# Kernel optimization log

Hardware: AMD Instinct MI355X
Metric: run time of the kernel (lower is better)

Reference implementation:

```python
import jax, jax.numpy as jnp
import numpy as np

LEVELS = 2
BS = 8                 # block_size == plane_h == plane_w
NORMALS = (0, 1, 2)    # axis-aligned plane normals within each block
TAU = 0.05
INV_SQRT2 = 0.7071067811865476

# ---------- 1D orthonormal Haar along an axis ----------

def _dwt1(x, axis):
    x = jnp.moveaxis(x, axis, -1)
    a, b = x[..., 0::2], x[..., 1::2]
    lo = (a + b) * INV_SQRT2
    hi = (a - b) * INV_SQRT2
    return jnp.moveaxis(lo, -1, axis), jnp.moveaxis(hi, -1, axis)


def _idwt1(lo, hi, axis):
    lo = jnp.moveaxis(lo, axis, -1)
    hi = jnp.moveaxis(hi, axis, -1)
    even = (lo + hi) * INV_SQRT2
    odd = (lo - hi) * INV_SQRT2
    y = jnp.stack([even, odd], axis=-1).reshape(lo.shape[:-1] + (lo.shape[-1] * 2,))
    return jnp.moveaxis(y, -1, axis)

# ---------- one level of separable 3D Haar (8 subbands) ----------

def _dwt3_level(x):
    ld, hd = _dwt1(x, -3)
    out = {}
    for dn, db in (('l', ld), ('h', hd)):
        lh, hh = _dwt1(db, -2)
        for hn, hb in (('l', lh), ('h', hh)):
            lw, hw = _dwt1(hb, -1)
            out[dn + hn + 'l'] = lw
            out[dn + hn + 'h'] = hw
    return out


def _idwt3_level(bands):
    rec_h = {dn + hn: _idwt1(bands[dn + hn + 'l'], bands[dn + hn + 'h'], -1)
             for dn in 'lh' for hn in 'lh'}
    rec_d = {dn: _idwt1(rec_h[dn + 'l'], rec_h[dn + 'h'], -2) for dn in 'lh'}
    return _idwt1(rec_d['l'], rec_d['h'], -3)

# ---------- full multi-level 2D Haar on the last two dims (planes) ----------

def _haar2_fwd(p):
    s = p.shape[-1]
    out = p
    while s > 1:
        sub = out[..., :s, :s]
        a, b = sub[..., 0::2, :], sub[..., 1::2, :]
        sub = jnp.concatenate([(a + b) * INV_SQRT2, (a - b) * INV_SQRT2], axis=-2)
        a, b = sub[..., :, 0::2], sub[..., :, 1::2]
        sub = jnp.concatenate([(a + b) * INV_SQRT2, (a - b) * INV_SQRT2], axis=-1)
        out = out.at[..., :s, :s].set(sub)
        s //= 2
    return out


def _haar2_inv(c):
    s_full = c.shape[-1]
    out = c
    s = 2
    while s <= s_full:
        sub = out[..., :s, :s]
        lo, hi = sub[..., :, :s // 2], sub[..., :, s // 2:]
        even = (lo + hi) * INV_SQRT2
        odd = (lo - hi) * INV_SQRT2
        sub = jnp.stack([even, odd], axis=-1).reshape(sub.shape[:-1] + (s,))
        lo, hi = sub[..., :s // 2, :], sub[..., s // 2:, :]
        even = (lo + hi) * INV_SQRT2
        odd = (lo - hi) * INV_SQRT2
        sub = jnp.stack([even, odd], axis=-2).reshape(sub.shape[:-2] + (s, s))
        out = out.at[..., :s, :s].set(sub)
        s *= 2
    return out

# ---------- block extraction / assembly ----------

def _extract_blocks(band, bs):
    B, C, D, H, W = band.shape
    pd, ph, pw = (-D) % bs, (-H) % bs, (-W) % bs
    band = jnp.pad(band, ((0, 0), (0, 0), (0, pd), (0, ph), (0, pw)), mode='edge')
    nd, nh, nw = (D + pd) // bs, (H + ph) // bs, (W + pw) // bs
    blk = band.reshape(B, C, nd, bs, nh, bs, nw, bs).transpose(0, 1, 2, 4, 6, 3, 5, 7)
    return blk.reshape(-1, bs, bs, bs), (B, C, D, H, W), (nd, nh, nw)


def _assemble_blocks(blocks, orig, nblk, bs):
    B, C, D, H, W = orig
    nd, nh, nw = nblk
    x = blocks.reshape(B, C, nd, nh, nw, bs, bs, bs).transpose(0, 1, 2, 5, 3, 6, 4, 7)
    x = x.reshape(B, C, nd * bs, nh * bs, nw * bs)
    return x[:, :, :D, :H, :W]

# ---------- planewise bandlet analysis / synthesis ----------

def _analyze(blocks):
    # for each normal axis n: slice cube into planes perpendicular to n, 2D Haar each plane
    return jnp.stack([_haar2_fwd(jnp.moveaxis(blocks, 1 + n, 1)) for n in NORMALS], axis=1)


def _synthesize(packed):
    recs = [jnp.moveaxis(_haar2_inv(packed[:, i]), 1, 1 + n) for i, n in enumerate(NORMALS)]
    acc = recs[0]
    for r in recs[1:]:
        acc = acc + r
    return acc / len(NORMALS)


def _soft_threshold(c, tau):
    dc = c[..., 0, 0]  # keep per-plane DC coefficient
    t = jnp.sign(c) * jnp.maximum(jnp.abs(c) - tau, 0.0)
    return t.at[..., 0, 0].set(dc)

# ---------- full encode -> threshold -> reconstruct ----------

def _forward(x):
    B, C, D, H, W = x.shape
    mult = 2 ** LEVELS
    pd, ph, pw = (-D) % mult, (-H) % mult, (-W) % mult
    xp = jnp.pad(x, ((0, 0), (0, 0), (0, pd), (0, ph), (0, pw)), mode='reflect')
    approx = xp
    levels = []
    for _ in range(LEVELS):
        bands = _dwt3_level(approx)
        approx = bands.pop('lll')
        levels.append(bands)
    rec_levels = []
    for bands in levels:
        rec = {}
        for name, band in bands.items():
            blocks, orig, nblk = _extract_blocks(band, BS)
            packed = _soft_threshold(_analyze(blocks), TAU)
            rec[name] = _assemble_blocks(_synthesize(packed), orig, nblk, BS)
        rec_levels.append(rec)
    y = approx
    for bands in reversed(rec_levels):
        bands = dict(bands)
        bands['lll'] = y
        y = _idwt3_level(bands)
    return y[:, :, :D, :H, :W]


def setup_inputs() -> dict:
    key = jax.random.key(0)
    x = jax.random.normal(key, (2, 1, 160, 160, 160), dtype=jnp.float32)
    return {"x": x}


def reference(x):
    return _forward(x)
```

## Files before the change

kernel.cpp:

```cpp
#include <hip/hip_runtime.h>

#define IS2 0.7071067811865476f
#define C3F 0.35355339059327373f
#define TAU_F 0.05f

__device__ __forceinline__ void haar2_fwd(float (&m)[64]) {
    float t[64];
    #pragma unroll
    for (int half = 4; half >= 1; half >>= 1) {
        const int sz = half * 2;
        #pragma unroll
        for (int r = 0; r < half; ++r)
            #pragma unroll
            for (int c = 0; c < sz; ++c) {
                float a = m[(2*r)*8 + c], b = m[(2*r+1)*8 + c];
                t[r*8 + c]        = (a + b) * IS2;
                t[(r+half)*8 + c] = (a - b) * IS2;
            }
        #pragma unroll
        for (int r = 0; r < sz; ++r)
            #pragma unroll
            for (int c = 0; c < sz; ++c) m[r*8+c] = t[r*8+c];
        #pragma unroll
        for (int r = 0; r < sz; ++r)
            #pragma unroll
            for (int c = 0; c < half; ++c) {
                float a = m[r*8 + 2*c], b = m[r*8 + 2*c + 1];
                t[r*8 + c]        = (a + b) * IS2;
                t[r*8 + c + half] = (a - b) * IS2;
            }
        #pragma unroll
        for (int r = 0; r < sz; ++r)
            #pragma unroll
            for (int c = 0; c < sz; ++c) m[r*8+c] = t[r*8+c];
    }
}

__device__ __forceinline__ void haar2_inv(float (&m)[64]) {
    float t[64];
    #pragma unroll
    for (int sz = 2; sz <= 8; sz <<= 1) {
        const int half = sz >> 1;
        #pragma unroll
        for (int r = 0; r < sz; ++r)
            #pragma unroll
            for (int c = 0; c < half; ++c) {
                float lo = m[r*8 + c], hi = m[r*8 + c + half];
                t[r*8 + 2*c]     = (lo + hi) * IS2;
                t[r*8 + 2*c + 1] = (lo - hi) * IS2;
            }
        #pragma unroll
        for (int r = 0; r < sz; ++r)
            #pragma unroll
            for (int c = 0; c < sz; ++c) m[r*8+c] = t[r*8+c];
        #pragma unroll
        for (int r = 0; r < half; ++r)
            #pragma unroll
            for (int c = 0; c < sz; ++c) {
                float lo = m[r*8 + c], hi = m[(r+half)*8 + c];
                t[(2*r)*8 + c]   = (lo + hi) * IS2;
                t[(2*r+1)*8 + c] = (lo - hi) * IS2;
            }
        #pragma unroll
        for (int r = 0; r < sz; ++r)
            #pragma unroll
            for (int c = 0; c < sz; ++c) m[r*8+c] = t[r*8+c];
    }
}

__device__ __forceinline__ void bandlet_slice(float (&m)[64]) {
    haar2_fwd(m);
    float dc = m[0];
    #pragma unroll
    for (int e = 0; e < 64; ++e) {
        float v = m[e];
        float av = fabsf(v) - TAU_F;
        m[e] = av > 0.0f ? copysignf(av, v) : 0.0f;
    }
    m[0] = dc;
    haar2_inv(m);
}

template<int S, int B>
__global__ __launch_bounds__(256) void dwt3_fwd(const float* __restrict__ in,
                                                float* __restrict__ out) {
    const int tid = blockIdx.x * blockDim.x + threadIdx.x;
    constexpr int total = B * S * S * S;
    if (tid >= total) return;
    const int w = tid % S;
    const int h = (tid / S) % S;
    const int d = (tid / (S*S)) % S;
    const int b = tid / (S*S*S);
    constexpr int IS = 2 * S;
    const float* p = in + (((size_t)b * IS + 2*d) * IS + 2*h) * IS + 2*w;

    float2 q00 = *(const float2*)(p);
    float2 q01 = *(const float2*)(p + IS);
    float2 q10 = *(const float2*)(p + (size_t)IS*IS);
    float2 q11 = *(const float2*)(p + (size_t)IS*IS + IS);

    float wl00 = q00.x + q00.y, wh00 = q00.x - q00.y;
    float wl01 = q01.x + q01.y, wh01 = q01.x - q01.y;
    float wl10 = q10.x + q10.y, wh10 = q10.x - q10.y;
    float wl11 = q11.x + q11.y, wh11 = q11.x - q11.y;
    float hl0l = wl00 + wl01, hh0l = wl00 - wl01;
    float hl0h = wh00 + wh01, hh0h = wh00 - wh01;
    float hl1l = wl10 + wl11, hh1l = wl10 - wl11;
    float hl1h = wh10 + wh11, hh1h = wh10 - wh11;
    constexpr size_t bs_ = (size_t)B * S * S * S;
    const size_t o = (size_t)tid;
    out[0*bs_ + o] = (hl0l + hl1l) * C3F;
    out[1*bs_ + o] = (hl0h + hl1h) * C3F;
    out[2*bs_ + o] = (hh0l + hh1l) * C3F;
    out[3*bs_ + o] = (hh0h + hh1h) * C3F;
    out[4*bs_ + o] = (hl0l - hl1l) * C3F;
    out[5*bs_ + o] = (hl0h - hl1h) * C3F;
    out[6*bs_ + o] = (hh0l - hh1l) * C3F;
    out[7*bs_ + o] = (hh0h - hh1h) * C3F;
}

template<int S, int B>
__global__ __launch_bounds__(256) void dwt3_inv(const float* __restrict__ bands,
                                                float* __restrict__ out) {
    const int tid = blockIdx.x * blockDim.x + threadIdx.x;
    constexpr int total = B * S * S * S;
    if (tid >= total) return;
    const int w = tid % S;
    const int h = (tid / S) % S;
    const int d = (tid / (S*S)) % S;
    const int b = tid / (S*S*S);
    constexpr size_t bs_ = (size_t)B * S * S * S;
    const size_t o = (size_t)tid;

    float b0 = bands[0*bs_+o], b1 = bands[1*bs_+o], b2 = bands[2*bs_+o], b3 = bands[3*bs_+o];
    float b4 = bands[4*bs_+o], b5 = bands[5*bs_+o], b6 = bands[6*bs_+o], b7 = bands[7*bs_+o];
    float c0 = b0 + b4, c1 = b1 + b5, c2 = b2 + b6, c3 = b3 + b7;
    float c4 = b0 - b4, c5 = b1 - b5, c6 = b2 - b6, c7 = b3 - b7;
    float e00 = c0 + c2, e01 = c1 + c3;
    float e02 = c0 - c2, e03 = c1 - c3;
    float e10 = c4 + c6, e11 = c5 + c7;
    float e12 = c4 - c6, e13 = c5 - c7;
    constexpr int IS = 2 * S;
    float* p = out + (((size_t)b * IS + 2*d) * IS + 2*h) * IS + 2*w;
    *(float2*)(p)                        = make_float2((e00+e01)*C3F, (e00-e01)*C3F);
    *(float2*)(p + IS)                   = make_float2((e02+e03)*C3F, (e02-e03)*C3F);
    *(float2*)(p + (size_t)IS*IS)        = make_float2((e10+e11)*C3F, (e10-e11)*C3F);
    *(float2*)(p + (size_t)IS*IS + IS)   = make_float2((e12+e13)*C3F, (e12-e13)*C3F);
}

__global__ __launch_bounds__(64, 2) void blockproc2(float* __restrict__ b1,
                                                    float* __restrict__ b2) {
    constexpr int LST = 516;
    __shared__ __align__(16) float lin[8 * LST];

    const int t  = threadIdx.x;
    const int nb = t >> 3;
    const int s  = t & 7;
    const int wg = blockIdx.x;

    float* base; unsigned S, BPB, ND; int bid; bool valid;
    if (wg < 1750) { base = b1; S = 80; BPB = 2000; ND = 10; bid = wg*8 + nb; valid = true; }
    else           { base = b2; S = 40; BPB = 250;  ND = 5;  bid = (wg-1750)*8 + nb; valid = bid < 1750; }

    const unsigned S2 = S * S, S3 = S2 * S;
    const unsigned ub   = (unsigned)bid;
    const unsigned band = ub / BPB;
    const unsigned r0   = ub - band * BPB;
    const unsigned nd2  = ND * ND, nd3 = nd2 * ND;
    const unsigned bb   = r0 / nd3;
    const unsigned r1   = r0 - bb * nd3;
    const unsigned di   = r1 / nd2;
    const unsigned r2i  = r1 - di * nd2;
    const unsigned hi   = r2i / ND;
    const unsigned wi   = r2i - hi * ND;
    float* gp = base + (size_t)band * (size_t)(2u * S3) + (size_t)bb * S3
              + (size_t)(8u * di) * S2 + (size_t)(8u * hi) * S + 8u * wi;

    float* L = &lin[nb * LST];

    if (valid) {
        #pragma unroll
        for (int u = 0; u < 8; ++u) {
            const float* g0 = gp + u * S2 + s * S;
            float4 v0 = *(const float4*)(g0);
            float4 v1 = *(const float4*)(g0 + 4);
            *(float4*)&L[u*64 + s*8]     = v0;
            *(float4*)&L[u*64 + s*8 + 4] = v1;
        }
    }
    __syncthreads();

    float a[64], g[64], w[64];

    #pragma unroll
    for (int r = 0; r < 8; ++r) {
        float4 v0 = *(const float4*)&L[s*64 + r*8];
        float4 v1 = *(const float4*)&L[s*64 + r*8 + 4];
        a[r*8+0]=v0.x; a[r*8+1]=v0.y; a[r*8+2]=v0.z; a[r*8+3]=v0.w;
        a[r*8+4]=v1.x; a[r*8+5]=v1.y; a[r*8+6]=v1.z; a[r*8+7]=v1.w;
    }
    bandlet_slice(a);

    #pragma unroll
    for (int r = 0; r < 8; ++r)
        #pragma unroll
        for (int c = 0; c < 8; ++c)
            g[r*8+c] = L[r*64 + c*8 + s];
    bandlet_slice(g);

    #pragma unroll
    for (int r = 0; r < 8; ++r) {
        float4 v0 = *(const float4*)&L[r*64 + s*8];
        float4 v1 = *(const float4*)&L[r*64 + s*8 + 4];
        w[r*8+0]=v0.x; w[r*8+1]=v0.y; w[r*8+2]=v0.z; w[r*8+3]=v0.w;
        w[r*8+4]=v1.x; w[r*8+5]=v1.y; w[r*8+6]=v1.z; w[r*8+7]=v1.w;
    }
    __syncthreads();

    #pragma unroll
    for (int r = 0; r < 8; ++r)
        #pragma unroll
        for (int c = 0; c < 8; ++c)
            L[r*64 + c*8 + s] = g[r*8+c];

    bandlet_slice(w);

    __syncthreads();
    #pragma unroll
    for (int r = 0; r < 8; ++r) {
        float4 v0 = *(const float4*)&L[s*64 + r*8];
        float4 v1 = *(const float4*)&L[s*64 + r*8 + 4];
        a[r*8+0]+=v0.x; a[r*8+1]+=v0.y; a[r*8+2]+=v0.z; a[r*8+3]+=v0.w;
        a[r*8+4]+=v1.x; a[r*8+5]+=v1.y; a[r*8+6]+=v1.z; a[r*8+7]+=v1.w;
    }
    __syncthreads();
    #pragma unroll
    for (int r = 0; r < 8; ++r) {
        float4 v0 = make_float4(w[r*8+0], w[r*8+1], w[r*8+2], w[r*8+3]);
        float4 v1 = make_float4(w[r*8+4], w[r*8+5], w[r*8+6], w[r*8+7]);
        *(float4*)&L[r*64 + s*8]     = v0;
        *(float4*)&L[r*64 + s*8 + 4] = v1;
    }
    __syncthreads();
    #pragma unroll
    for (int r = 0; r < 8; ++r) {
        float4 v0 = *(const float4*)&L[s*64 + r*8];
        float4 v1 = *(const float4*)&L[s*64 + r*8 + 4];
        a[r*8+0]+=v0.x; a[r*8+1]+=v0.y; a[r*8+2]+=v0.z; a[r*8+3]+=v0.w;
        a[r*8+4]+=v1.x; a[r*8+5]+=v1.y; a[r*8+6]+=v1.z; a[r*8+7]+=v1.w;
    }

    if (valid) {
        #pragma unroll
        for (int j = 0; j < 8; ++j) {
            float4 o0 = make_float4(a[j*8+0]*(1.0f/3.0f), a[j*8+1]*(1.0f/3.0f),
                                    a[j*8+2]*(1.0f/3.0f), a[j*8+3]*(1.0f/3.0f));
            float4 o1 = make_float4(a[j*8+4]*(1.0f/3.0f), a[j*8+5]*(1.0f/3.0f),
                                    a[j*8+6]*(1.0f/3.0f), a[j*8+7]*(1.0f/3.0f));
            float* q = gp + s * S2 + j * S;
            *(float4*)(q)     = o0;
            *(float4*)(q + 4) = o1;
        }
    }
}

extern "C" void kernel_launch(void* const* d_in, const int* in_sizes, int n_in,
                              void* d_out, int out_size, void* d_ws, size_t ws_size,
                              hipStream_t stream) {
    const float* x = (const float*)d_in[0];
    float* out = (float*)d_out;
    float* bands1 = (float*)d_ws;
    float* bands2 = (float*)d_out;

    constexpr int B = 2;
    constexpr size_t B1S = (size_t)B * 80 * 80 * 80;
    constexpr size_t B2S = (size_t)B * 40 * 40 * 40;

    dwt3_fwd<80, B><<<(B*80*80*80) / 256, 256, 0, stream>>>(x, bands1);
    dwt3_fwd<40, B><<<(B*40*40*40) / 256, 256, 0, stream>>>(bands1, bands2);
    blockproc2<<<1750 + 219, 64, 0, stream>>>(bands1 + B1S, bands2 + B2S);
    dwt3_inv<40, B><<<(B*40*40*40) / 256, 256, 0, stream>>>(bands2, bands1);
    dwt3_inv<80, B><<<(B*80*80*80) / 256, 256, 0, stream>>>(bands1, out);
}
```

Before: 119.2 us.

## Fuse forward DWT with bandlet processing and collapse level-2 into one kernel

Level-1 forward Haar is fused with the bandlet thresholding of its seven detail bands in shared memory, so the detail bands are processed without a global round trip first. The whole level-2 path (forward DWT, bandlet processing, inverse DWT) becomes a single kernel operating in place on the LLL band. This cuts five launches to three and removes several full global-memory passes. The cost is small 64-thread workgroups with 7/8 lanes active in the bandlet stage, and only 250 workgroups for level 2, which may leave the GPU underoccupied.

```diff
diff --git a/kernel.cpp b/kernel.cpp
--- a/kernel.cpp
+++ b/kernel.cpp
@@ -81,55 +81,227 @@
     haar2_inv(m);
 }
 
-template<int S, int B>
-__global__ __launch_bounds__(256) void dwt3_fwd(const float* __restrict__ in,
-                                                float* __restrict__ out) {
+__device__ __forceinline__ void bandlet_core(float* __restrict__ L, int s,
+                                             bool valid, float (&a)[64]) {
+    float g[64], w[64];
+    if (valid) {
+        #pragma unroll
+        for (int r = 0; r < 8; ++r) {
+            float4 v0 = *(const float4*)&L[s*64 + r*8];
+            float4 v1 = *(const float4*)&L[s*64 + r*8 + 4];
+            a[r*8+0]=v0.x; a[r*8+1]=v0.y; a[r*8+2]=v0.z; a[r*8+3]=v0.w;
+            a[r*8+4]=v1.x; a[r*8+5]=v1.y; a[r*8+6]=v1.z; a[r*8+7]=v1.w;
+        }
+        bandlet_slice(a);
+        #pragma unroll
+        for (int r = 0; r < 8; ++r)
+            #pragma unroll
+            for (int c = 0; c < 8; ++c)
+                g[r*8+c] = L[r*64 + c*8 + s];
+        bandlet_slice(g);
+        #pragma unroll
+        for (int r = 0; r < 8; ++r) {
+            float4 v0 = *(const float4*)&L[r*64 + s*8];
+            float4 v1 = *(const float4*)&L[r*64 + s*8 + 4];
+            w[r*8+0]=v0.x; w[r*8+1]=v0.y; w[r*8+2]=v0.z; w[r*8+3]=v0.w;
+            w[r*8+4]=v1.x; w[r*8+5]=v1.y; w[r*8+6]=v1.z; w[r*8+7]=v1.w;
+        }
+    }
+    __syncthreads();
+    if (valid) {
+        #pragma unroll
+        for (int r = 0; r < 8; ++r)
+            #pragma unroll
+            for (int c = 0; c < 8; ++c)
+                L[r*64 + c*8 + s] = g[r*8+c];
+        bandlet_slice(w);
+    }
+    __syncthreads();
+    if (valid) {
+        #pragma unroll
+        for (int r = 0; r < 8; ++r) {
+            float4 v0 = *(const float4*)&L[s*64 + r*8];
+            float4 v1 = *(const float4*)&L[s*64 + r*8 + 4];
+            a[r*8+0]+=v0.x; a[r*8+1]+=v0.y; a[r*8+2]+=v0.z; a[r*8+3]+=v0.w;
+            a[r*8+4]+=v1.x; a[r*8+5]+=v1.y; a[r*8+6]+=v1.z; a[r*8+7]+=v1.w;
+        }
+    }
+    __syncthreads();
+    if (valid) {
+        #pragma unroll
+        for (int r = 0; r < 8; ++r) {
+            *(float4*)&L[r*64 + s*8]     = make_float4(w[r*8+0], w[r*8+1], w[r*8+2], w[r*8+3]);
+            *(float4*)&L[r*64 + s*8 + 4] = make_float4(w[r*8+4], w[r*8+5], w[r*8+6], w[r*8+7]);
+        }
+    }
+    __syncthreads();
+    if (valid) {
+        #pragma unroll
+        for (int r = 0; r < 8; ++r) {
+            float4 v0 = *(const float4*)&L[s*64 + r*8];
+            float4 v1 = *(const float4*)&L[s*64 + r*8 + 4];
+            a[r*8+0]+=v0.x; a[r*8+1]+=v0.y; a[r*8+2]+=v0.z; a[r*8+3]+=v0.w;
+            a[r*8+4]+=v1.x; a[r*8+5]+=v1.y; a[r*8+6]+=v1.z; a[r*8+7]+=v1.w;
+        }
+    }
+}
+
+__global__ __launch_bounds__(64, 2) void fwd1_bp(const float* __restrict__ x,
+                                                 float* __restrict__ bands) {
+    constexpr int LST = 516;
+    constexpr size_t B1S = (size_t)2 * 80 * 80 * 80;
+    __shared__ __align__(16) float lin[7 * LST];
+
+    const int t  = threadIdx.x;
+    const int wg = blockIdx.x;
+    const int b  = wg / 1000;
+    const int tl = wg - b * 1000;
+    const int td = tl / 100;
+    const int rr = tl - td * 100;
+    const int th = rr / 10;
+    const int tw = rr - th * 10;
+    const int j = t >> 3, w = t & 7;
+
+    const float* ip = x + ((size_t)(b*160 + 16*td)) * 25600 + (size_t)(16*th) * 160 + 16*tw;
+    float* lllp = bands + ((size_t)(b*80 + 8*td)) * 6400 + (size_t)(8*th) * 80 + 8*tw;
+
+    #pragma unroll
+    for (int q = 0; q < 8; ++q) {
+        const float* p = ip + (size_t)(2*q) * 25600 + (2*j) * 160 + 2*w;
+        float2 q00 = *(const float2*)(p);
+        float2 q01 = *(const float2*)(p + 160);
+        float2 q10 = *(const float2*)(p + 25600);
+        float2 q11 = *(const float2*)(p + 25600 + 160);
+        float wl00 = q00.x + q00.y, wh00 = q00.x - q00.y;
+        float wl01 = q01.x + q01.y, wh01 = q01.x - q01.y;
+        float wl10 = q10.x + q10.y, wh10 = q10.x - q10.y;
+        float wl11 = q11.x + q11.y, wh11 = q11.x - q11.y;
+        float hl0l = wl00 + wl01, hh0l = wl00 - wl01;
+        float hl0h = wh00 + wh01, hh0h = wh00 - wh01;
+        float hl1l = wl10 + wl11, hh1l = wl10 - wl11;
+        float hl1h = wh10 + wh11, hh1h = wh10 - wh11;
+        const int pos = q*64 + j*8 + w;
+        lin[0*LST + pos] = (hl0h + hl1h) * C3F;
+        lin[1*LST + pos] = (hh0l + hh1l) * C3F;
+        lin[2*LST + pos] = (hh0h + hh1h) * C3F;
+        lin[3*LST + pos] = (hl0l - hl1l) * C3F;
+        lin[4*LST + pos] = (hl0h - hl1h) * C3F;
+        lin[5*LST + pos] = (hh0l - hh1l) * C3F;
+        lin[6*LST + pos] = (hh0h - hh1h) * C3F;
+        lllp[q*6400 + j*80 + w] = (hl0l + hl1l) * C3F;
+    }
+    __syncthreads();
+
+    const int nbp = t >> 3, s = t & 7;
+    const bool valid = nbp < 7;
+    float a[64];
+    bandlet_core(&lin[(valid ? nbp : 0) * LST], s, valid, a);
+
+    if (valid) {
+        float* gp = bands + (size_t)(nbp + 1) * B1S
+                  + ((size_t)(b*80 + 8*td + s)) * 6400 + (size_t)(8*th) * 80 + 8*tw;
+        #pragma unroll
+        for (int jj = 0; jj < 8; ++jj) {
+            float* qo = gp + jj * 80;
+            *(float4*)(qo)     = make_float4(a[jj*8+0]*(1.0f/3.0f), a[jj*8+1]*(1.0f/3.0f),
+                                             a[jj*8+2]*(1.0f/3.0f), a[jj*8+3]*(1.0f/3.0f));
+            *(float4*)(qo + 4) = make_float4(a[jj*8+4]*(1.0f/3.0f), a[jj*8+5]*(1.0f/3.0f),
+                                             a[jj*8+6]*(1.0f/3.0f), a[jj*8+7]*(1.0f/3.0f));
+        }
+    }
+}
+
+__global__ __launch_bounds__(64, 2) void l2_pipeline(float* __restrict__ lll) {
+    constexpr int LST = 516;
+    __shared__ __align__(16) float lin[8 * LST];
+
+    const int t  = threadIdx.x;
+    const int wg = blockIdx.x;
+    const int b  = wg / 125;
+    const int tl = wg - b * 125;
+    const int td = tl / 25;
+    const int rr = tl - td * 25;
+    const int th = rr / 5;
+    const int tw = rr - th * 5;
+    const int j = t >> 3, w = t & 7;
+
+    float* base = lll + ((size_t)(b*80 + 16*td)) * 6400 + (size_t)(16*th) * 80 + 16*tw;
+
+    #pragma unroll
+    for (int q = 0; q < 8; ++q) {
+        const float* p = base + (size_t)(2*q) * 6400 + (2*j) * 80 + 2*w;
+        float2 q00 = *(const float2*)(p);
+        float2 q01 = *(const float2*)(p + 80);
+        float2 q10 = *(const float2*)(p + 6400);
+        float2 q11 = *(const float2*)(p + 6400 + 80);
+        float wl00 = q00.x + q00.y, wh00 = q00.x - q00.y;
+        float wl01 = q01.x + q01.y, wh01 = q01.x - q01.y;
+        float wl10 = q10.x + q10.y, wh10 = q10.x - q10.y;
+        float wl11 = q11.x + q11.y, wh11 = q11.x - q11.y;
+        float hl0l = wl00 + wl01, hh0l = wl00 - wl01;
+        float hl0h = wh00 + wh01, hh0h = wh00 - wh01;
+        float hl1l = wl10 + wl11, hh1l = wl10 - wl11;
+        float hl1h = wh10 + wh11, hh1h = wh10 - wh11;
+        const int pos = q*64 + j*8 + w;
+        lin[0*LST + pos] = (hl0l + hl1l) * C3F;
+        lin[1*LST + pos] = (hl0h + hl1h) * C3F;
+        lin[2*LST + pos] = (hh0l + hh1l) * C3F;
+        lin[3*LST + pos] = (hh0h + hh1h) * C3F;
+        lin[4*LST + pos] = (hl0l - hl1l) * C3F;
+        lin[5*LST + pos] = (hl0h - hl1h) * C3F;
+        lin[6*LST + pos] = (hh0l - hh1l) * C3F;
+        lin[7*LST + pos] = (hh0h - hh1h) * C3F;
+    }
+    __syncthreads();
+
+    const int nbp = t >> 3, s = t & 7;
+    const bool valid = nbp < 7;
+    float a[64];
+    bandlet_core(&lin[(valid ? nbp + 1 : 0) * LST], s, valid, a);
+
+    __syncthreads();
+    if (valid) {
+        float* L = &lin[(nbp + 1) * LST];
+        #pragma unroll
+        for (int jj = 0; jj < 8; ++jj) {
+            *(float4*)&L[s*64 + jj*8]     = make_float4(a[jj*8+0]*(1.0f/3.0f), a[jj*8+1]*(1.0f/3.0f),
+                                                        a[jj*8+2]*(1.0f/3.0f), a[jj*8+3]*(1.0f/3.0f));
+            *(float4*)&L[s*64 + jj*8 + 4] = make_float4(a[jj*8+4]*(1.0f/3.0f), a[jj*8+5]*(1.0f/3.0f),
+                                                        a[jj*8+6]*(1.0f/3.0f), a[jj*8+7]*(1.0f/3.0f));
+        }
+    }
+    __syncthreads();
+
+    #pragma unroll
+    for (int q = 0; q < 8; ++q) {
+        const int pos = q*64 + j*8 + w;
+        float b0 = lin[0*LST + pos], b1 = lin[1*LST + pos];
+        float b2 = lin[2*LST + pos], b3 = lin[3*LST + pos];
+        float b4 = lin[4*LST + pos], b5 = lin[5*LST + pos];
+        float b6 = lin[6*LST + pos], b7 = lin[7*LST + pos];
+        float c0 = b0 + b4, c1 = b1 + b5, c2 = b2 + b6, c3 = b3 + b7;
+        float c4 = b0 - b4, c5 = b1 - b5, c6 = b2 - b6, c7 = b3 - b7;
+        float e00 = c0 + c2, e01 = c1 + c3;
+        float e02 = c0 - c2, e03 = c1 - c3;
+        float e10 = c4 + c6, e11 = c5 + c7;
+        float e12 = c4 - c6, e13 = c5 - c7;
+        float* pp = base + (size_t)(2*q) * 6400 + (2*j) * 80 + 2*w;
+        *(float2*)(pp)             = make_float2((e00+e01)*C3F, (e00-e01)*C3F);
+        *(float2*)(pp + 80)        = make_float2((e02+e03)*C3F, (e02-e03)*C3F);
+        *(float2*)(pp + 6400)      = make_float2((e10+e11)*C3F, (e10-e11)*C3F);
+        *(float2*)(pp + 6400 + 80) = make_float2((e12+e13)*C3F, (e12-e13)*C3F);
+    }
+}
+
+__global__ __launch_bounds__(256) void dwt3_inv80(const float* __restrict__ bands,
+                                                  float* __restrict__ out) {
     const int tid = blockIdx.x * blockDim.x + threadIdx.x;
-    constexpr int total = B * S * S * S;
-    if (tid >= total) return;
+    constexpr int S = 80;
     const int w = tid % S;
     const int h = (tid / S) % S;
     const int d = (tid / (S*S)) % S;
     const int b = tid / (S*S*S);
-    constexpr int IS = 2 * S;
-    const float* p = in + (((size_t)b * IS + 2*d) * IS + 2*h) * IS + 2*w;
-
-    float2 q00 = *(const float2*)(p);
-    float2 q01 = *(const float2*)(p + IS);
-    float2 q10 = *(const float2*)(p + (size_t)IS*IS);
-    float2 q11 = *(const float2*)(p + (size_t)IS*IS + IS);
-
-    float wl00 = q00.x + q00.y, wh00 = q00.x - q00.y;
-    float wl01 = q01.x + q01.y, wh01 = q01.x - q01.y;
-    float wl10 = q10.x + q10.y, wh10 = q10.x - q10.y;
-    float wl11 = q11.x + q11.y, wh11 = q11.x - q11.y;
-    float hl0l = wl00 + wl01, hh0l = wl00 - wl01;
-    float hl0h = wh00 + wh01, hh0h = wh00 - wh01;
-    float hl1l = wl10 + wl11, hh1l = wl10 - wl11;
-    float hl1h = wh10 + wh11, hh1h = wh10 - wh11;
-    constexpr size_t bs_ = (size_t)B * S * S * S;
-    const size_t o = (size_t)tid;
-    out[0*bs_ + o] = (hl0l + hl1l) * C3F;
-    out[1*bs_ + o] = (hl0h + hl1h) * C3F;
-    out[2*bs_ + o] = (hh0l + hh1l) * C3F;
-    out[3*bs_ + o] = (hh0h + hh1h) * C3F;
-    out[4*bs_ + o] = (hl0l - hl1l) * C3F;
-    out[5*bs_ + o] = (hl0h - hl1h) * C3F;
-    out[6*bs_ + o] = (hh0l - hh1l) * C3F;
-    out[7*bs_ + o] = (hh0h - hh1h) * C3F;
-}
-
-template<int S, int B>
-__global__ __launch_bounds__(256) void dwt3_inv(const float* __restrict__ bands,
-                                                float* __restrict__ out) {
-    const int tid = blockIdx.x * blockDim.x + threadIdx.x;
-    constexpr int total = B * S * S * S;
-    if (tid >= total) return;
-    const int w = tid % S;
-    const int h = (tid / S) % S;
-    const int d = (tid / (S*S)) % S;
-    const int b = tid / (S*S*S);
-    constexpr size_t bs_ = (size_t)B * S * S * S;
+    constexpr size_t bs_ = (size_t)2 * S * S * S;
     const size_t o = (size_t)tid;
 
     float b0 = bands[0*bs_+o], b1 = bands[1*bs_+o], b2 = bands[2*bs_+o], b3 = bands[3*bs_+o];
@@ -142,126 +314,10 @@
     float e12 = c4 - c6, e13 = c5 - c7;
     constexpr int IS = 2 * S;
     float* p = out + (((size_t)b * IS + 2*d) * IS + 2*h) * IS + 2*w;
-    *(float2*)(p)                        = make_float2((e00+e01)*C3F, (e00-e01)*C3F);
-    *(float2*)(p + IS)                   = make_float2((e02+e03)*C3F, (e02-e03)*C3F);
-    *(float2*)(p + (size_t)IS*IS)        = make_float2((e10+e11)*C3F, (e10-e11)*C3F);
-    *(float2*)(p + (size_t)IS*IS + IS)   = make_float2((e12+e13)*C3F, (e12-e13)*C3F);
-}
-
-__global__ __launch_bounds__(64, 2) void blockproc2(float* __restrict__ b1,
-                                                    float* __restrict__ b2) {
-    constexpr int LST = 516;
-    __shared__ __align__(16) float lin[8 * LST];
-
-    const int t  = threadIdx.x;
-    const int nb = t >> 3;
-    const int s  = t & 7;
-    const int wg = blockIdx.x;
-
-    float* base; unsigned S, BPB, ND; int bid; bool valid;
-    if (wg < 1750) { base = b1; S = 80; BPB = 2000; ND = 10; bid = wg*8 + nb; valid = true; }
-    else           { base = b2; S = 40; BPB = 250;  ND = 5;  bid = (wg-1750)*8 + nb; valid = bid < 1750; }
-
-    const unsigned S2 = S * S, S3 = S2 * S;
-    const unsigned ub   = (unsigned)bid;
-    const unsigned band = ub / BPB;
-    const unsigned r0   = ub - band * BPB;
-    const unsigned nd2  = ND * ND, nd3 = nd2 * ND;
-    const unsigned bb   = r0 / nd3;
-    const unsigned r1   = r0 - bb * nd3;
-    const unsigned di   = r1 / nd2;
-    const unsigned r2i  = r1 - di * nd2;
-    const unsigned hi   = r2i / ND;
-    const unsigned wi   = r2i - hi * ND;
-    float* gp = base + (size_t)band * (size_t)(2u * S3) + (size_t)bb * S3
-              + (size_t)(8u * di) * S2 + (size_t)(8u * hi) * S + 8u * wi;
-
-    float* L = &lin[nb * LST];
-
-    if (valid) {
-        #pragma unroll
-        for (int u = 0; u < 8; ++u) {
-            const float* g0 = gp + u * S2 + s * S;
-            float4 v0 = *(const float4*)(g0);
-            float4 v1 = *(const float4*)(g0 + 4);
-            *(float4*)&L[u*64 + s*8]     = v0;
-            *(float4*)&L[u*64 + s*8 + 4] = v1;
-        }
-    }
-    __syncthreads();
-
-    float a[64], g[64], w[64];
-
-    #pragma unroll
-    for (int r = 0; r < 8; ++r) {
-        float4 v0 = *(const float4*)&L[s*64 + r*8];
-        float4 v1 = *(const float4*)&L[s*64 + r*8 + 4];
-        a[r*8+0]=v0.x; a[r*8+1]=v0.y; a[r*8+2]=v0.z; a[r*8+3]=v0.w;
-        a[r*8+4]=v1.x; a[r*8+5]=v1.y; a[r*8+6]=v1.z; a[r*8+7]=v1.w;
-    }
-    bandlet_slice(a);
-
-    #pragma unroll
-    for (int r = 0; r < 8; ++r)
-        #pragma unroll
-        for (int c = 0; c < 8; ++c)
-            g[r*8+c] = L[r*64 + c*8 + s];
-    bandlet_slice(g);
-
-    #pragma unroll
-    for (int r = 0; r < 8; ++r) {
-        float4 v0 = *(const float4*)&L[r*64 + s*8];
-        float4 v1 = *(const float4*)&L[r*64 + s*8 + 4];
-        w[r*8+0]=v0.x; w[r*8+1]=v0.y; w[r*8+2]=v0.z; w[r*8+3]=v0.w;
-        w[r*8+4]=v1.x; w[r*8+5]=v1.y; w[r*8+6]=v1.z; w[r*8+7]=v1.w;
-    }
-    __syncthreads();
-
-    #pragma unroll
-    for (int r = 0; r < 8; ++r)
-        #pragma unroll
-        for (int c = 0; c < 8; ++c)
-            L[r*64 + c*8 + s] = g[r*8+c];
-
-    bandlet_slice(w);
-
-    __syncthreads();
-    #pragma unroll
-    for (int r = 0; r < 8; ++r) {
-        float4 v0 = *(const float4*)&L[s*64 + r*8];
-        float4 v1 = *(const float4*)&L[s*64 + r*8 + 4];
-        a[r*8+0]+=v0.x; a[r*8+1]+=v0.y; a[r*8+2]+=v0.z; a[r*8+3]+=v0.w;
-        a[r*8+4]+=v1.x; a[r*8+5]+=v1.y; a[r*8+6]+=v1.z; a[r*8+7]+=v1.w;
-    }
-    __syncthreads();
-    #pragma unroll
-    for (int r = 0; r < 8; ++r) {
-        float4 v0 = make_float4(w[r*8+0], w[r*8+1], w[r*8+2], w[r*8+3]);
-        float4 v1 = make_float4(w[r*8+4], w[r*8+5], w[r*8+6], w[r*8+7]);
-        *(float4*)&L[r*64 + s*8]     = v0;
-        *(float4*)&L[r*64 + s*8 + 4] = v1;
-    }
-    __syncthreads();
-    #pragma unroll
-    for (int r = 0; r < 8; ++r) {
-        float4 v0 = *(const float4*)&L[s*64 + r*8];
-        float4 v1 = *(const float4*)&L[s*64 + r*8 + 4];
-        a[r*8+0]+=v0.x; a[r*8+1]+=v0.y; a[r*8+2]+=v0.z; a[r*8+3]+=v0.w;
-        a[r*8+4]+=v1.x; a[r*8+5]+=v1.y; a[r*8+6]+=v1.z; a[r*8+7]+=v1.w;
-    }
-
-    if (valid) {
-        #pragma unroll
-        for (int j = 0; j < 8; ++j) {
-            float4 o0 = make_float4(a[j*8+0]*(1.0f/3.0f), a[j*8+1]*(1.0f/3.0f),
-                                    a[j*8+2]*(1.0f/3.0f), a[j*8+3]*(1.0f/3.0f));
-            float4 o1 = make_float4(a[j*8+4]*(1.0f/3.0f), a[j*8+5]*(1.0f/3.0f),
-                                    a[j*8+6]*(1.0f/3.0f), a[j*8+7]*(1.0f/3.0f));
-            float* q = gp + s * S2 + j * S;
-            *(float4*)(q)     = o0;
-            *(float4*)(q + 4) = o1;
-        }
-    }
+    *(float2*)(p)                      = make_float2((e00+e01)*C3F, (e00-e01)*C3F);
+    *(float2*)(p + IS)                 = make_float2((e02+e03)*C3F, (e02-e03)*C3F);
+    *(float2*)(p + (size_t)IS*IS)      = make_float2((e10+e11)*C3F, (e10-e11)*C3F);
+    *(float2*)(p + (size_t)IS*IS + IS) = make_float2((e12+e13)*C3F, (e12-e13)*C3F);
 }
 
 extern "C" void kernel_launch(void* const* d_in, const int* in_sizes, int n_in,
@@ -269,16 +325,9 @@
                               hipStream_t stream) {
     const float* x = (const float*)d_in[0];
     float* out = (float*)d_out;
-    float* bands1 = (float*)d_ws;
-    float* bands2 = (float*)d_out;
-
-    constexpr int B = 2;
-    constexpr size_t B1S = (size_t)B * 80 * 80 * 80;
-    constexpr size_t B2S = (size_t)B * 40 * 40 * 40;
-
-    dwt3_fwd<80, B><<<(B*80*80*80) / 256, 256, 0, stream>>>(x, bands1);
-    dwt3_fwd<40, B><<<(B*40*40*40) / 256, 256, 0, stream>>>(bands1, bands2);
-    blockproc2<<<1750 + 219, 64, 0, stream>>>(bands1 + B1S, bands2 + B2S);
-    dwt3_inv<40, B><<<(B*40*40*40) / 256, 256, 0, stream>>>(bands2, bands1);
-    dwt3_inv<80, B><<<(B*80*80*80) / 256, 256, 0, stream>>>(bands1, out);
-}
+    float* bands = (float*)d_ws;
+
+    fwd1_bp<<<2000, 64, 0, stream>>>(x, bands);
+    l2_pipeline<<<250, 64, 0, stream>>>(bands);
+    dwt3_inv80<<<4000, 256, 0, stream>>>(bands, out);
+}
```

After: 117.1 us. Within noise of the previous version (-1.8%).
